# Optimization experiments

Hardware: AMD Instinct MI355X
Metric: run time of the kernel (lower is better)

The kernel has to match this reference:

```python
import jax, jax.numpy as jnp
import numpy as np

BLOCK_SIZE = 64
IN_CHANNELS = 1024
OUT_CHANNELS = 1024
O_NBLOCKS = OUT_CHANNELS // BLOCK_SIZE  # 16
I_NBLOCKS = IN_CHANNELS // BLOCK_SIZE   # 16
N_TOKENS = 32768


def setup_inputs() -> dict:
    key = jax.random.key(0)
    kx, kw = jax.random.split(key)
    x = jax.random.normal(kx, (N_TOKENS, IN_CHANNELS), dtype=jnp.float32)
    # xavier_uniform over the (o_nblocks, i_nblocks, block_size) tensor:
    # fan_in = i_nblocks * block_size, fan_out = block_size (last-dim convention)
    fan_in = I_NBLOCKS * BLOCK_SIZE
    fan_out = BLOCK_SIZE
    limit = float(np.sqrt(6.0 / (fan_in + fan_out)))
    w = jax.random.uniform(kw, (O_NBLOCKS, I_NBLOCKS, BLOCK_SIZE),
                           dtype=jnp.float32, minval=-limit, maxval=limit)
    return {"x": x, "w": w}


def _build_dense_weight(w):
    # w: (R, Q, bs). Dense W[r*bs+i, q*bs+j] = w[r, q, (i - j) mod bs]
    R, Q, bs = w.shape
    i = jnp.arange(bs)
    idx = (i[:, None] - i[None, :]) % bs          # (bs, bs) circulant index
    Wb = w[:, :, idx]                              # (R, Q, bs, bs)
    return Wb.transpose(0, 2, 1, 3).reshape(R * bs, Q * bs)  # (out, in)


def reference(x, w):
    W = _build_dense_weight(w)                     # (out_channels, in_channels)
    return x @ W.T                                 # F.linear, no bias
```

## Files before the change

### kernel.cpp

```cpp
#include <hip/hip_runtime.h>
#include <stdint.h>


#define NTOK 32768
#define NCH  1024
#define BK   64
#define NKT  (NCH / BK)

typedef short bf16x8 __attribute__((ext_vector_type(8)));
typedef float f32x4  __attribute__((ext_vector_type(4)));
typedef unsigned short u16x8 __attribute__((ext_vector_type(8)));

static __device__ __forceinline__ unsigned short f2bf(float f) {
    unsigned int u = __float_as_uint(f);
    u += 0x7FFFu + ((u >> 16) & 1u);
    return (unsigned short)(u >> 16);
}

#define GLOAD16(gp, lp)                                                          \
    __builtin_amdgcn_global_load_lds(                                            \
        (const __attribute__((address_space(1))) unsigned int*)(gp),             \
        (__attribute__((address_space(3))) unsigned int*)(lp), 16, 0, 0)

__global__ void cvt_x_kernel(const float* __restrict__ x, unsigned short* __restrict__ xb) {
    int i = blockIdx.x * blockDim.x + threadIdx.x;
    int row = i >> 7;
    int j   = i & 127;
    const float4* src = (const float4*)(x + (((size_t)row) << 10) + (j << 3));
    float4 a = src[0], b = src[1];
    u16x8 v;
    v[0]=f2bf(a.x); v[1]=f2bf(a.y); v[2]=f2bf(a.z); v[3]=f2bf(a.w);
    v[4]=f2bf(b.x); v[5]=f2bf(b.y); v[6]=f2bf(b.z); v[7]=f2bf(b.w);
    int js = (j & ~7) | ((j & 7) ^ (row & 7));
    *(u16x8*)(xb + (((size_t)row) << 10) + (js << 3)) = v;
}

__global__ void build_w_kernel(const float* __restrict__ w, unsigned short* __restrict__ Wb) {
    int i = blockIdx.x * blockDim.x + threadIdx.x;
    int o = i >> 7;
    int j = i & 127;
    int r = o >> 6;
    int q = j >> 3;
    const float* wrow = w + ((r * 16 + q) << 6);
    int k0 = j << 3;
    u16x8 v;
#pragma unroll
    for (int e = 0; e < 8; ++e) v[e] = f2bf(wrow[(o - (k0 + e)) & 63]);
    int js = (j & ~7) | ((j & 7) ^ (o & 7));
    *(u16x8*)(Wb + (((size_t)o) << 10) + (js << 3)) = v;
}

#define PHASE_BAR() __builtin_amdgcn_s_barrier()
#define LGKM0() asm volatile("s_waitcnt lgkmcnt(0)" ::: "memory")
#define VMCNT(n) asm volatile("s_waitcnt vmcnt(" #n ")" ::: "memory")
#define SETPRIO(n) __builtin_amdgcn_s_setprio(n)
#define MFMA4(d, av, bv) d = __builtin_amdgcn_mfma_f32_16x16x32_bf16(av, bv, d, 0, 0, 0)

#define STAGE_HALF(src, ldsbuf, t, h) do {                                       \
    const char* _s = (src) + (((size_t)(h)) << 18) + (((size_t)(t)) << 7);       \
    char* _d = (ldsbuf) + ((h) << 14) + (wv << 10);                              \
    GLOAD16(_s, _d);                                                             \
    GLOAD16(_s + ((size_t)64 << 11), _d + 8192);                                 \
} while (0)

#define NOSTG ((void)0)

#define KTILE(Abuf, Bbuf, S1, S2, S3, S4, W4)                                    \
  do {                                                                           \
    bf16x8 afr[4][2], bfr[4][2];                                                 \
    _Pragma("unroll") for (int m = 0; m < 4; ++m)                                \
      _Pragma("unroll") for (int ks = 0; ks < 2; ++ks)                           \
        afr[m][ks] = *(const bf16x8*)((Abuf) + a_off[ks] + m * 2048);            \
    _Pragma("unroll") for (int n = 0; n < 2; ++n)                                \
      _Pragma("unroll") for (int ks = 0; ks < 2; ++ks)                           \
        bfr[n][ks] = *(const bf16x8*)((Bbuf) + b_off[ks] + n * 2048);            \
    S1;                                                                          \
    PHASE_BAR(); LGKM0();                                                        \
    SETPRIO(1);                                                                  \
    _Pragma("unroll") for (int m = 0; m < 4; ++m)                                \
      _Pragma("unroll") for (int n = 0; n < 2; ++n) {                            \
        MFMA4(acc[m][n], afr[m][0], bfr[n][0]);                                  \
        MFMA4(acc[m][n], afr[m][1], bfr[n][1]);                                  \
      }                                                                          \
    SETPRIO(0); PHASE_BAR();                                                     \
                                                                         \
    _Pragma("unroll") for (int n = 2; n < 4; ++n)                                \
      _Pragma("unroll") for (int ks = 0; ks < 2; ++ks)                           \
        bfr[n][ks] = *(const bf16x8*)((Bbuf) + b_off[ks] + n * 2048);            \
    S2;                                                                          \
    PHASE_BAR(); LGKM0();                                                        \
    SETPRIO(1);                                                                  \
    _Pragma("unroll") for (int m = 0; m < 4; ++m)                                \
      _Pragma("unroll") for (int n = 2; n < 4; ++n) {                            \
        MFMA4(acc[m][n], afr[m][0], bfr[n][0]);                                  \
        MFMA4(acc[m][n], afr[m][1], bfr[n][1]);                                  \
      }                                                                          \
    SETPRIO(0); PHASE_BAR();                                                     \
                                                                         \
    _Pragma("unroll") for (int m = 0; m < 4; ++m)                                \
      _Pragma("unroll") for (int ks = 0; ks < 2; ++ks)                           \
        afr[m][ks] = *(const bf16x8*)((Abuf) + a_off[ks] + (m + 4) * 2048);      \
    S3;                                                                          \
    PHASE_BAR(); LGKM0();                                                        \
    SETPRIO(1);                                                                  \
    _Pragma("unroll") for (int m = 0; m < 4; ++m)                                \
      _Pragma("unroll") for (int n = 0; n < 2; ++n) {                            \
        MFMA4(acc[m + 4][n], afr[m][0], bfr[n][0]);                              \
        MFMA4(acc[m + 4][n], afr[m][1], bfr[n][1]);                              \
      }                                                                          \
    SETPRIO(0); PHASE_BAR();                                                     \
                                                                         \
    S4; W4;                                                                      \
    PHASE_BAR();                                                                 \
    SETPRIO(1);                                                                  \
    _Pragma("unroll") for (int m = 0; m < 4; ++m)                                \
      _Pragma("unroll") for (int n = 2; n < 4; ++n) {                            \
        MFMA4(acc[m + 4][n], afr[m][0], bfr[n][0]);                              \
        MFMA4(acc[m + 4][n], afr[m][1], bfr[n][1]);                              \
      }                                                                          \
    SETPRIO(0); PHASE_BAR();                                                     \
  } while (0)

__global__ void __launch_bounds__(512, 1) gemm8_kernel(const unsigned short* __restrict__ A,
                                                       const unsigned short* __restrict__ B,
                                                       float* __restrict__ C) {
    __shared__ __align__(16) char lds[131072];
    char* As0 = lds;
    char* As1 = lds + 32768;
    char* Bs0 = lds + 65536;
    char* Bs1 = lds + 98304;

    int tid  = threadIdx.x;
    int lane = tid & 63;
    int wv   = tid >> 6;
    int wr   = wv >> 2;
    int wc   = wv & 3;

    int cpx = gridDim.x >> 3;
    int wid = ((int)blockIdx.x & 7) * cpx + ((int)blockIdx.x >> 3);
    int tn = wid & 3, tm = wid >> 2;
    int m0 = tm * 256, n0 = tn * 256;

    const char* srcA = (const char*)A + (((size_t)(m0 + (tid >> 3))) << 11) + ((tid & 7) << 4);
    const char* srcB = (const char*)B + (((size_t)(n0 + (tid >> 3))) << 11) + ((tid & 7) << 4);

    int xr   = (lane & 7) << 4;
    int kq16 = (lane >> 4) << 4;
    int a_off[2], b_off[2];
    {
        int arow = ((wr << 7) + (lane & 15)) << 7;
        int brow = ((wc << 6) + (lane & 15)) << 7;
        a_off[0] = arow + ((kq16 + 0)  ^ xr);
        a_off[1] = arow + ((kq16 + 64) ^ xr);
        b_off[0] = brow + ((kq16 + 0)  ^ xr);
        b_off[1] = brow + ((kq16 + 64) ^ xr);
    }

    f32x4 acc[8][4] = {};

    STAGE_HALF(srcA, As0, 0, 0); STAGE_HALF(srcA, As0, 0, 1);
    STAGE_HALF(srcB, Bs0, 0, 0); STAGE_HALF(srcB, Bs0, 0, 1);
    STAGE_HALF(srcB, Bs1, 1, 0); STAGE_HALF(srcB, Bs1, 1, 1);
    VMCNT(4); PHASE_BAR();

    for (int t = 0; t < NKT - 2; t += 2) {
        KTILE(As0, Bs0,
              STAGE_HALF(srcA, As1, t + 1, 0),
              STAGE_HALF(srcA, As1, t + 1, 1),
              STAGE_HALF(srcB, Bs0, t + 2, 0),
              STAGE_HALF(srcB, Bs0, t + 2, 1),
              VMCNT(4));
        KTILE(As1, Bs1,
              STAGE_HALF(srcA, As0, t + 2, 0),
              STAGE_HALF(srcA, As0, t + 2, 1),
              STAGE_HALF(srcB, Bs1, t + 3, 0),
              STAGE_HALF(srcB, Bs1, t + 3, 1),
              VMCNT(4));
    }
    KTILE(As0, Bs0,
          STAGE_HALF(srcA, As1, NKT - 1, 0),
          STAGE_HALF(srcA, As1, NKT - 1, 1),
          NOSTG, NOSTG, VMCNT(0));
    KTILE(As1, Bs1, NOSTG, NOSTG, NOSTG, NOSTG, NOSTG);

    float* Cp = C + ((size_t)(m0 + wr * 128)) * NCH + n0 + wc * 64;
    int cc = lane & 15;
    int rr = (lane >> 4) << 2;
#pragma unroll
    for (int m = 0; m < 8; ++m)
#pragma unroll
        for (int j = 0; j < 4; ++j) {
            float* rowp = Cp + ((size_t)(m * 16 + rr + j)) * NCH;
#pragma unroll
            for (int n = 0; n < 4; ++n)
                rowp[n * 16 + cc] = acc[m][n][j];
        }
}

__global__ void naive_kernel(const float* __restrict__ x, const float* __restrict__ w,
                             float* __restrict__ out) {
    int t = blockIdx.x;
    int o = blockIdx.y * 256 + threadIdx.x;
    const float* xr = x + (size_t)t * NCH;
    int r = o >> 6, oi = o & 63;
    float s = 0.f;
    for (int q = 0; q < 16; ++q) {
        const float* wq = w + (r * 16 + q) * 64;
        const float* xq = xr + q * 64;
#pragma unroll 8
        for (int j = 0; j < 64; ++j) s += xq[j] * wq[(oi - j) & 63];
    }
    out[(size_t)t * NCH + o] = s;
}

extern "C" void kernel_launch(void* const* d_in, const int* in_sizes, int n_in,
                              void* d_out, int out_size, void* d_ws, size_t ws_size,
                              hipStream_t stream) {
    const float* x = (const float*)d_in[0];
    const float* w = (const float*)d_in[1];
    float* out = (float*)d_out;

    const size_t needX = (size_t)NTOK * NCH * sizeof(unsigned short);
    const size_t needW = (size_t)NCH * NCH * sizeof(unsigned short);

    if (ws_size >= needX + needW) {
        unsigned short* xb = (unsigned short*)d_ws;
        unsigned short* Wb = (unsigned short*)((char*)d_ws + needX);
        hipLaunchKernelGGL(cvt_x_kernel, dim3(NTOK * 128 / 256), dim3(256), 0, stream, x, xb);
        hipLaunchKernelGGL(build_w_kernel, dim3(NCH * 128 / 256), dim3(256), 0, stream, w, Wb);
        hipLaunchKernelGGL(gemm8_kernel, dim3(512), dim3(512), 0, stream, xb, Wb, out);
    } else {
        hipLaunchKernelGGL(naive_kernel, dim3(NTOK, 4), dim3(256), 0, stream, x, w, out);
    }
}
```

Before: 114.1 us.

## Fuse fp32-to-bf16 conversion of X into GEMM A-tile staging

Removes the separate cvt_x pass that wrote a bf16 copy of X to workspace. The GEMM now loads fp32 X rows into registers one K-tile ahead, converts them to bf16 and writes swizzled tiles into LDS, while B still uses direct global-to-LDS loads. This avoids writing and re-reading the bf16 X buffer and one kernel launch. In exchange, the GEMM reads twice as many bytes for A, uses more registers per thread, and adds conversion ALU work and hand-tuned vmcnt waits inside the pipelined loop.

```diff
diff --git a/kernel.cpp b/kernel.cpp
--- a/kernel.cpp
+++ b/kernel.cpp
@@ -17,23 +17,17 @@
     return (unsigned short)(u >> 16);
 }
 
+static __device__ __forceinline__ u16x8 pack8(float4 a, float4 b) {
+    u16x8 v;
+    v[0]=f2bf(a.x); v[1]=f2bf(a.y); v[2]=f2bf(a.z); v[3]=f2bf(a.w);
+    v[4]=f2bf(b.x); v[5]=f2bf(b.y); v[6]=f2bf(b.z); v[7]=f2bf(b.w);
+    return v;
+}
+
 #define GLOAD16(gp, lp)                                                          \
     __builtin_amdgcn_global_load_lds(                                            \
         (const __attribute__((address_space(1))) unsigned int*)(gp),             \
         (__attribute__((address_space(3))) unsigned int*)(lp), 16, 0, 0)
-
-__global__ void cvt_x_kernel(const float* __restrict__ x, unsigned short* __restrict__ xb) {
-    int i = blockIdx.x * blockDim.x + threadIdx.x;
-    int row = i >> 7;
-    int j   = i & 127;
-    const float4* src = (const float4*)(x + (((size_t)row) << 10) + (j << 3));
-    float4 a = src[0], b = src[1];
-    u16x8 v;
-    v[0]=f2bf(a.x); v[1]=f2bf(a.y); v[2]=f2bf(a.z); v[3]=f2bf(a.w);
-    v[4]=f2bf(b.x); v[5]=f2bf(b.y); v[6]=f2bf(b.z); v[7]=f2bf(b.w);
-    int js = (j & ~7) | ((j & 7) ^ (row & 7));
-    *(u16x8*)(xb + (((size_t)row) << 10) + (js << 3)) = v;
-}
 
 __global__ void build_w_kernel(const float* __restrict__ w, unsigned short* __restrict__ Wb) {
     int i = blockIdx.x * blockDim.x + threadIdx.x;
@@ -53,19 +47,40 @@
 #define PHASE_BAR() __builtin_amdgcn_s_barrier()
 #define LGKM0() asm volatile("s_waitcnt lgkmcnt(0)" ::: "memory")
 #define VMCNT(n) asm volatile("s_waitcnt vmcnt(" #n ")" ::: "memory")
+#define CFENCE() asm volatile("" ::: "memory")
 #define SETPRIO(n) __builtin_amdgcn_s_setprio(n)
 #define MFMA4(d, av, bv) d = __builtin_amdgcn_mfma_f32_16x16x32_bf16(av, bv, d, 0, 0, 0)
 
-#define STAGE_HALF(src, ldsbuf, t, h) do {                                       \
-    const char* _s = (src) + (((size_t)(h)) << 18) + (((size_t)(t)) << 7);       \
+#define STAGE_HALF_B(ldsbuf, t, h) do {                                          \
+    const char* _s = srcB + (((size_t)(h)) << 18) + (((size_t)(t)) << 7);        \
     char* _d = (ldsbuf) + ((h) << 14) + (wv << 10);                              \
     GLOAD16(_s, _d);                                                             \
     GLOAD16(_s + ((size_t)64 << 11), _d + 8192);                                 \
 } while (0)
 
-#define NOSTG ((void)0)
-
-#define KTILE(Abuf, Bbuf, S1, S2, S3, S4, W4)                                    \
+#define ISSUE_A(t) do {                                                          \
+    const float4* _p0 = (const float4*)(pA + ((t) << 6));                        \
+    const float4* _p1 = (const float4*)(pA + ((t) << 6) + (128 << 10));          \
+    areg[0]=_p0[0]; areg[1]=_p0[1]; areg[2]=_p0[2]; areg[3]=_p0[3];              \
+    areg[4]=_p1[0]; areg[5]=_p1[1]; areg[6]=_p1[2]; areg[7]=_p1[3];              \
+    CFENCE();                                                                    \
+} while (0)
+
+#define WRITE_A(Abuf) do {                                                       \
+    u16x8 _w0 = pack8(areg[0], areg[1]);                                         \
+    u16x8 _w1 = pack8(areg[2], areg[3]);                                         \
+    u16x8 _w2 = pack8(areg[4], areg[5]);                                         \
+    u16x8 _w3 = pack8(areg[6], areg[7]);                                         \
+    *(u16x8*)((Abuf) + aw0)         = _w0;                                       \
+    *(u16x8*)((Abuf) + aw1)         = _w1;                                       \
+    *(u16x8*)((Abuf) + aw0 + 16384) = _w2;                                       \
+    *(u16x8*)((Abuf) + aw1 + 16384) = _w3;                                       \
+    CFENCE();                                                                    \
+} while (0)
+
+#define NOHOOK ((void)0)
+
+#define KTILE(Abuf, Bbuf, H3, H4)                                                \
   do {                                                                           \
     bf16x8 afr[4][2], bfr[4][2];                                                 \
     _Pragma("unroll") for (int m = 0; m < 4; ++m)                                \
@@ -74,7 +89,6 @@
     _Pragma("unroll") for (int n = 0; n < 2; ++n)                                \
       _Pragma("unroll") for (int ks = 0; ks < 2; ++ks)                           \
         bfr[n][ks] = *(const bf16x8*)((Bbuf) + b_off[ks] + n * 2048);            \
-    S1;                                                                          \
     PHASE_BAR(); LGKM0();                                                        \
     SETPRIO(1);                                                                  \
     _Pragma("unroll") for (int m = 0; m < 4; ++m)                                \
@@ -87,7 +101,6 @@
     _Pragma("unroll") for (int n = 2; n < 4; ++n)                                \
       _Pragma("unroll") for (int ks = 0; ks < 2; ++ks)                           \
         bfr[n][ks] = *(const bf16x8*)((Bbuf) + b_off[ks] + n * 2048);            \
-    S2;                                                                          \
     PHASE_BAR(); LGKM0();                                                        \
     SETPRIO(1);                                                                  \
     _Pragma("unroll") for (int m = 0; m < 4; ++m)                                \
@@ -100,7 +113,7 @@
     _Pragma("unroll") for (int m = 0; m < 4; ++m)                                \
       _Pragma("unroll") for (int ks = 0; ks < 2; ++ks)                           \
         afr[m][ks] = *(const bf16x8*)((Abuf) + a_off[ks] + (m + 4) * 2048);      \
-    S3;                                                                          \
+    H3;                                                                          \
     PHASE_BAR(); LGKM0();                                                        \
     SETPRIO(1);                                                                  \
     _Pragma("unroll") for (int m = 0; m < 4; ++m)                                \
@@ -110,7 +123,7 @@
       }                                                                          \
     SETPRIO(0); PHASE_BAR();                                                     \
                                                                          \
-    S4; W4;                                                                      \
+    H4;                                                                          \
     PHASE_BAR();                                                                 \
     SETPRIO(1);                                                                  \
     _Pragma("unroll") for (int m = 0; m < 4; ++m)                                \
@@ -121,7 +134,7 @@
     SETPRIO(0); PHASE_BAR();                                                     \
   } while (0)
 
-__global__ void __launch_bounds__(512, 1) gemm8_kernel(const unsigned short* __restrict__ A,
+__global__ void __launch_bounds__(512, 1) gemm8_kernel(const float* __restrict__ X,
                                                        const unsigned short* __restrict__ B,
                                                        float* __restrict__ C) {
     __shared__ __align__(16) char lds[131072];
@@ -141,8 +154,16 @@
     int tn = wid & 3, tm = wid >> 2;
     int m0 = tm * 256, n0 = tn * 256;
 
-    const char* srcA = (const char*)A + (((size_t)(m0 + (tid >> 3))) << 11) + ((tid & 7) << 4);
     const char* srcB = (const char*)B + (((size_t)(n0 + (tid >> 3))) << 11) + ((tid & 7) << 4);
+
+    const float* pA = X + ((size_t)(m0 + (tid >> 2)) << 10) + ((tid & 3) << 4);
+    float4 areg[8];
+
+    int wrow = tid >> 2;
+    int j0   = (tid & 3) << 1;
+    int r7   = wrow & 7;
+    int aw0  = wrow * 128 + (((j0    ) ^ r7) << 4);
+    int aw1  = wrow * 128 + (((j0 + 1) ^ r7) << 4);
 
     int xr   = (lane & 7) << 4;
     int kq16 = (lane >> 4) << 4;
@@ -158,30 +179,28 @@
 
     f32x4 acc[8][4] = {};
 
-    STAGE_HALF(srcA, As0, 0, 0); STAGE_HALF(srcA, As0, 0, 1);
-    STAGE_HALF(srcB, Bs0, 0, 0); STAGE_HALF(srcB, Bs0, 0, 1);
-    STAGE_HALF(srcB, Bs1, 1, 0); STAGE_HALF(srcB, Bs1, 1, 1);
-    VMCNT(4); PHASE_BAR();
+    ISSUE_A(0);
+    STAGE_HALF_B(Bs0, 0, 0); STAGE_HALF_B(Bs0, 0, 1);
+    VMCNT(4);
+    WRITE_A(As0);
+    ISSUE_A(1);
+    STAGE_HALF_B(Bs1, 1, 0); STAGE_HALF_B(Bs1, 1, 1);
+    VMCNT(12);
+    LGKM0();
+    PHASE_BAR();
 
     for (int t = 0; t < NKT - 2; t += 2) {
         KTILE(As0, Bs0,
-              STAGE_HALF(srcA, As1, t + 1, 0),
-              STAGE_HALF(srcA, As1, t + 1, 1),
-              STAGE_HALF(srcB, Bs0, t + 2, 0),
-              STAGE_HALF(srcB, Bs0, t + 2, 1),
-              VMCNT(4));
+              { STAGE_HALF_B(Bs0, t + 2, 0); STAGE_HALF_B(Bs0, t + 2, 1);
+                VMCNT(4); WRITE_A(As1); },
+              { ISSUE_A(t + 2); });
         KTILE(As1, Bs1,
-              STAGE_HALF(srcA, As0, t + 2, 0),
-              STAGE_HALF(srcA, As0, t + 2, 1),
-              STAGE_HALF(srcB, Bs1, t + 3, 0),
-              STAGE_HALF(srcB, Bs1, t + 3, 1),
-              VMCNT(4));
-    }
-    KTILE(As0, Bs0,
-          STAGE_HALF(srcA, As1, NKT - 1, 0),
-          STAGE_HALF(srcA, As1, NKT - 1, 1),
-          NOSTG, NOSTG, VMCNT(0));
-    KTILE(As1, Bs1, NOSTG, NOSTG, NOSTG, NOSTG, NOSTG);
+              { STAGE_HALF_B(Bs1, t + 3, 0); STAGE_HALF_B(Bs1, t + 3, 1);
+                VMCNT(4); WRITE_A(As0); },
+              { ISSUE_A(t + 3); });
+    }
+    KTILE(As0, Bs0, { VMCNT(0); WRITE_A(As1); }, NOHOOK);
+    KTILE(As1, Bs1, NOHOOK, NOHOOK);
 
     float* Cp = C + ((size_t)(m0 + wr * 128)) * NCH + n0 + wc * 64;
     int cc = lane & 15;
@@ -220,15 +239,12 @@
     const float* w = (const float*)d_in[1];
     float* out = (float*)d_out;
 
-    const size_t needX = (size_t)NTOK * NCH * sizeof(unsigned short);
     const size_t needW = (size_t)NCH * NCH * sizeof(unsigned short);
 
-    if (ws_size >= needX + needW) {
-        unsigned short* xb = (unsigned short*)d_ws;
-        unsigned short* Wb = (unsigned short*)((char*)d_ws + needX);
-        hipLaunchKernelGGL(cvt_x_kernel, dim3(NTOK * 128 / 256), dim3(256), 0, stream, x, xb);
+    if (ws_size >= needW) {
+        unsigned short* Wb = (unsigned short*)d_ws;
         hipLaunchKernelGGL(build_w_kernel, dim3(NCH * 128 / 256), dim3(256), 0, stream, w, Wb);
-        hipLaunchKernelGGL(gemm8_kernel, dim3(512), dim3(512), 0, stream, xb, Wb, out);
+        hipLaunchKernelGGL(gemm8_kernel, dim3(512), dim3(512), 0, stream, x, Wb, out);
     } else {
         hipLaunchKernelGGL(naive_kernel, dim3(NTOK, 4), dim3(256), 0, stream, x, w, out);
     }
```

After: 122.7 us. +7.5%, slower.

## Shrink GEMM tile to 128x128 with simpler double-buffered k-loop and higher occupancy

Applied to the files above, without the earlier changes.

Replaces the 256x256 tile GEMM, which used a hand-scheduled four-phase k-tile with staggered half-stage loads, with a 128x128 tile kernel. The new kernel uses plain double buffering with one full-drain wait per k-step, 64 KB of LDS, and launch bounds allowing 4 blocks per CU across 2048 blocks. The intent is to hide latency through occupancy instead of intra-block phase scheduling. The cost is lower data reuse per tile, so more global and LDS traffic per flop, and the loss of the fine-grained overlap in the old schedule.

```diff
diff --git a/kernel.cpp b/kernel.cpp
--- a/kernel.cpp
+++ b/kernel.cpp
@@ -52,83 +52,47 @@
 
 #define PHASE_BAR() __builtin_amdgcn_s_barrier()
 #define LGKM0() asm volatile("s_waitcnt lgkmcnt(0)" ::: "memory")
-#define VMCNT(n) asm volatile("s_waitcnt vmcnt(" #n ")" ::: "memory")
+#define VMCNT0() asm volatile("s_waitcnt vmcnt(0)" ::: "memory")
 #define SETPRIO(n) __builtin_amdgcn_s_setprio(n)
 #define MFMA4(d, av, bv) d = __builtin_amdgcn_mfma_f32_16x16x32_bf16(av, bv, d, 0, 0, 0)
+#define NOHOOK ((void)0)
 
-#define STAGE_HALF(src, ldsbuf, t, h) do {                                       \
-    const char* _s = (src) + (((size_t)(h)) << 18) + (((size_t)(t)) << 7);       \
-    char* _d = (ldsbuf) + ((h) << 14) + (wv << 10);                              \
-    GLOAD16(_s, _d);                                                             \
-    GLOAD16(_s + ((size_t)64 << 11), _d + 8192);                                 \
+#define STAGE(bufA, bufB, t) do {                                                \
+    const char* _sa = srcA + ((t) << 7);                                         \
+    const char* _sb = srcB + ((t) << 7);                                         \
+    char* _da = (bufA) + (wv << 10);                                             \
+    char* _db = (bufB) + (wv << 10);                                             \
+    GLOAD16(_sa, _da); GLOAD16(_sa + (64 << 11), _da + 8192);                    \
+    GLOAD16(_sb, _db); GLOAD16(_sb + (64 << 11), _db + 8192);                    \
 } while (0)
 
-#define NOSTG ((void)0)
-
-#define KTILE(Abuf, Bbuf, S1, S2, S3, S4, W4)                                    \
-  do {                                                                           \
-    bf16x8 afr[4][2], bfr[4][2];                                                 \
+#define KSTEP(Abuf, Bbuf, DO_STAGE) do {                                         \
+    DO_STAGE;                                                                    \
+    bf16x8 afr[4][2], bfr[2][2];                                                 \
     _Pragma("unroll") for (int m = 0; m < 4; ++m)                                \
       _Pragma("unroll") for (int ks = 0; ks < 2; ++ks)                           \
         afr[m][ks] = *(const bf16x8*)((Abuf) + a_off[ks] + m * 2048);            \
     _Pragma("unroll") for (int n = 0; n < 2; ++n)                                \
       _Pragma("unroll") for (int ks = 0; ks < 2; ++ks)                           \
         bfr[n][ks] = *(const bf16x8*)((Bbuf) + b_off[ks] + n * 2048);            \
-    S1;                                                                          \
-    PHASE_BAR(); LGKM0();                                                        \
+    LGKM0();                                                                     \
     SETPRIO(1);                                                                  \
     _Pragma("unroll") for (int m = 0; m < 4; ++m)                                \
       _Pragma("unroll") for (int n = 0; n < 2; ++n) {                            \
         MFMA4(acc[m][n], afr[m][0], bfr[n][0]);                                  \
         MFMA4(acc[m][n], afr[m][1], bfr[n][1]);                                  \
       }                                                                          \
-    SETPRIO(0); PHASE_BAR();                                                     \
-                                                                         \
-    _Pragma("unroll") for (int n = 2; n < 4; ++n)                                \
-      _Pragma("unroll") for (int ks = 0; ks < 2; ++ks)                           \
-        bfr[n][ks] = *(const bf16x8*)((Bbuf) + b_off[ks] + n * 2048);            \
-    S2;                                                                          \
-    PHASE_BAR(); LGKM0();                                                        \
-    SETPRIO(1);                                                                  \
-    _Pragma("unroll") for (int m = 0; m < 4; ++m)                                \
-      _Pragma("unroll") for (int n = 2; n < 4; ++n) {                            \
-        MFMA4(acc[m][n], afr[m][0], bfr[n][0]);                                  \
-        MFMA4(acc[m][n], afr[m][1], bfr[n][1]);                                  \
-      }                                                                          \
-    SETPRIO(0); PHASE_BAR();                                                     \
-                                                                         \
-    _Pragma("unroll") for (int m = 0; m < 4; ++m)                                \
-      _Pragma("unroll") for (int ks = 0; ks < 2; ++ks)                           \
-        afr[m][ks] = *(const bf16x8*)((Abuf) + a_off[ks] + (m + 4) * 2048);      \
-    S3;                                                                          \
-    PHASE_BAR(); LGKM0();                                                        \
-    SETPRIO(1);                                                                  \
-    _Pragma("unroll") for (int m = 0; m < 4; ++m)                                \
-      _Pragma("unroll") for (int n = 0; n < 2; ++n) {                            \
-        MFMA4(acc[m + 4][n], afr[m][0], bfr[n][0]);                              \
-        MFMA4(acc[m + 4][n], afr[m][1], bfr[n][1]);                              \
-      }                                                                          \
-    SETPRIO(0); PHASE_BAR();                                                     \
-                                                                         \
-    S4; W4;                                                                      \
-    PHASE_BAR();                                                                 \
-    SETPRIO(1);                                                                  \
-    _Pragma("unroll") for (int m = 0; m < 4; ++m)                                \
-      _Pragma("unroll") for (int n = 2; n < 4; ++n) {                            \
-        MFMA4(acc[m + 4][n], afr[m][0], bfr[n][0]);                              \
-        MFMA4(acc[m + 4][n], afr[m][1], bfr[n][1]);                              \
-      }                                                                          \
-    SETPRIO(0); PHASE_BAR();                                                     \
-  } while (0)
+    SETPRIO(0);                                                                  \
+} while (0)
 
-__global__ void __launch_bounds__(512, 1) gemm8_kernel(const unsigned short* __restrict__ A,
-                                                       const unsigned short* __restrict__ B,
-                                                       float* __restrict__ C) {
-    __shared__ __align__(16) char lds[131072];
+__global__ void __launch_bounds__(512, 4) gemm128_kernel(const unsigned short* __restrict__ A,
+                                                         const unsigned short* __restrict__ B,
+                                                         float* __restrict__ C) {
+    __shared__ __align__(16) char lds[65536];
     char* As0 = lds;
-    char* As1 = lds + 32768;
-    char* Bs0 = lds + 65536;
-    char* Bs1 = lds + 98304;
+    char* As1 = lds + 16384;
+    char* Bs0 = lds + 32768;
+    char* Bs1 = lds + 49152;
 
     int tid  = threadIdx.x;
     int lane = tid & 63;
@@ -138,61 +102,45 @@
 
     int cpx = gridDim.x >> 3;
     int wid = ((int)blockIdx.x & 7) * cpx + ((int)blockIdx.x >> 3);
-    int tn = wid & 3, tm = wid >> 2;
-    int m0 = tm * 256, n0 = tn * 256;
+    int tn = wid & 7, tm = wid >> 3;
+    int m0 = tm * 128, n0 = tn * 128;
 
     const char* srcA = (const char*)A + (((size_t)(m0 + (tid >> 3))) << 11) + ((tid & 7) << 4);
     const char* srcB = (const char*)B + (((size_t)(n0 + (tid >> 3))) << 11) + ((tid & 7) << 4);
 
-    int xr   = (lane & 7) << 4;
+    int xa   = (lane & 7) << 4;
     int kq16 = (lane >> 4) << 4;
-    int a_off[2], b_off[2];
-    {
-        int arow = ((wr << 7) + (lane & 15)) << 7;
-        int brow = ((wc << 6) + (lane & 15)) << 7;
-        a_off[0] = arow + ((kq16 + 0)  ^ xr);
-        a_off[1] = arow + ((kq16 + 64) ^ xr);
-        b_off[0] = brow + ((kq16 + 0)  ^ xr);
-        b_off[1] = brow + ((kq16 + 64) ^ xr);
+    int abase = (wr * 64 + (lane & 15)) * 128;
+    int bbase = (wc * 32 + (lane & 15)) * 128;
+    int a_off[2] = { abase + (kq16 ^ xa), abase + ((64 + kq16) ^ xa) };
+    int b_off[2] = { bbase + (kq16 ^ xa), bbase + ((64 + kq16) ^ xa) };
+
+    f32x4 acc[4][2] = {};
+
+    STAGE(As0, Bs0, 0);
+    VMCNT0(); PHASE_BAR();
+
+    for (int t = 0; t < NKT; t += 2) {
+        KSTEP(As0, Bs0, STAGE(As1, Bs1, t + 1));
+        VMCNT0(); PHASE_BAR();
+        if (t + 2 < NKT) {
+            KSTEP(As1, Bs1, STAGE(As0, Bs0, t + 2));
+            VMCNT0(); PHASE_BAR();
+        } else {
+            KSTEP(As1, Bs1, NOHOOK);
+        }
     }
 
-    f32x4 acc[8][4] = {};
-
-    STAGE_HALF(srcA, As0, 0, 0); STAGE_HALF(srcA, As0, 0, 1);
-    STAGE_HALF(srcB, Bs0, 0, 0); STAGE_HALF(srcB, Bs0, 0, 1);
-    STAGE_HALF(srcB, Bs1, 1, 0); STAGE_HALF(srcB, Bs1, 1, 1);
-    VMCNT(4); PHASE_BAR();
-
-    for (int t = 0; t < NKT - 2; t += 2) {
-        KTILE(As0, Bs0,
-              STAGE_HALF(srcA, As1, t + 1, 0),
-              STAGE_HALF(srcA, As1, t + 1, 1),
-              STAGE_HALF(srcB, Bs0, t + 2, 0),
-              STAGE_HALF(srcB, Bs0, t + 2, 1),
-              VMCNT(4));
-        KTILE(As1, Bs1,
-              STAGE_HALF(srcA, As0, t + 2, 0),
-              STAGE_HALF(srcA, As0, t + 2, 1),
-              STAGE_HALF(srcB, Bs1, t + 3, 0),
-              STAGE_HALF(srcB, Bs1, t + 3, 1),
-              VMCNT(4));
-    }
-    KTILE(As0, Bs0,
-          STAGE_HALF(srcA, As1, NKT - 1, 0),
-          STAGE_HALF(srcA, As1, NKT - 1, 1),
-          NOSTG, NOSTG, VMCNT(0));
-    KTILE(As1, Bs1, NOSTG, NOSTG, NOSTG, NOSTG, NOSTG);
-
-    float* Cp = C + ((size_t)(m0 + wr * 128)) * NCH + n0 + wc * 64;
+    float* Cp = C + ((size_t)(m0 + wr * 64)) * NCH + n0 + wc * 32;
     int cc = lane & 15;
     int rr = (lane >> 4) << 2;
 #pragma unroll
-    for (int m = 0; m < 8; ++m)
+    for (int m = 0; m < 4; ++m)
 #pragma unroll
         for (int j = 0; j < 4; ++j) {
             float* rowp = Cp + ((size_t)(m * 16 + rr + j)) * NCH;
 #pragma unroll
-            for (int n = 0; n < 4; ++n)
+            for (int n = 0; n < 2; ++n)
                 rowp[n * 16 + cc] = acc[m][n][j];
         }
 }
@@ -228,7 +176,7 @@
         unsigned short* Wb = (unsigned short*)((char*)d_ws + needX);
         hipLaunchKernelGGL(cvt_x_kernel, dim3(NTOK * 128 / 256), dim3(256), 0, stream, x, xb);
         hipLaunchKernelGGL(build_w_kernel, dim3(NCH * 128 / 256), dim3(256), 0, stream, w, Wb);
-        hipLaunchKernelGGL(gemm8_kernel, dim3(512), dim3(512), 0, stream, xb, Wb, out);
+        hipLaunchKernelGGL(gemm128_kernel, dim3(2048), dim3(512), 0, stream, xb, Wb, out);
     } else {
         hipLaunchKernelGGL(naive_kernel, dim3(NTOK, 4), dim3(256), 0, stream, x, w, out);
     }
```

Result: faster. 111.4 us (-2.4%).
